# Kernel optimization log

Hardware: AMD Instinct MI355X
Metric: run time of the kernel (lower is better)

Reference implementation:

```python
import jax, jax.numpy as jnp
import numpy as np

G = 8          # deformable groups
K = 9          # 3x3 kernel points
MAXR = 10.0    # max_residue_magnitude


def conv2d(x, w, b):
    # x: [B,Cin,H,W], w: [Cout,Cin,3,3], SAME padding, stride 1
    y = jax.lax.conv_general_dilated(x, w, (1, 1), ((1, 1), (1, 1)),
                                     dimension_numbers=('NCHW', 'OIHW', 'NCHW'))
    return y + b[None, :, None, None]


def lrelu(x):
    return jnp.where(x >= 0, x, 0.1 * x)


def offset_branch(x, ws, bs):
    for w, b in zip(ws[:-1], bs[:-1]):
        x = lrelu(conv2d(x, w, b))
    return conv2d(x, ws[-1], bs[-1])


def mdcn(x, offset, mask, w, b):
    # Modulated deformable conv, 3x3, stride 1, pad 1, dilation 1, groups=1.
    # offset: [B, G*K*2, H, W] ordered (g, k, (y,x)); mask: [B, G*K, H, W]
    B, C, H, W = x.shape
    Cg = C // G
    off = offset.reshape(B, G, K, 2, H, W)
    m = mask.reshape(B, G, K, H, W)
    ky = (jnp.arange(K) // 3 - 1).astype(x.dtype)   # kernel dy, pad=1
    kx = (jnp.arange(K) % 3 - 1).astype(x.dtype)    # kernel dx
    hy = jnp.arange(H, dtype=x.dtype)
    wx = jnp.arange(W, dtype=x.dtype)
    py = hy[None, None, None, :, None] + ky[None, None, :, None, None] + off[:, :, :, 0]  # [B,G,K,H,W]
    px = wx[None, None, None, None, :] + kx[None, None, :, None, None] + off[:, :, :, 1]
    y0f = jnp.floor(py); x0f = jnp.floor(px)
    ly = py - y0f; lx = px - x0f
    y0 = y0f.astype(jnp.int32); x0 = x0f.astype(jnp.int32)
    xf = x.reshape(B, G, Cg, H * W)

    def gather(yi, xi):
        valid = ((yi >= 0) & (yi < H) & (xi >= 0) & (xi < W)).astype(x.dtype)
        yc = jnp.clip(yi, 0, H - 1)
        xc = jnp.clip(xi, 0, W - 1)
        idx = (yc * W + xc).reshape(B, G, 1, K * H * W)
        v = jnp.take_along_axis(xf, idx, axis=3).reshape(B, G, Cg, K, H, W)
        return v * valid.reshape(B, G, 1, K, H, W)

    ly_ = ly[:, :, None]; lx_ = lx[:, :, None]  # [B,G,1,K,H,W]
    samp = (gather(y0, x0) * (1 - ly_) * (1 - lx_)
            + gather(y0, x0 + 1) * (1 - ly_) * lx_
            + gather(y0 + 1, x0) * ly_ * (1 - lx_)
            + gather(y0 + 1, x0 + 1) * ly_ * lx_)
    samp = samp * m[:, :, None]                 # modulation
    wr = w.reshape(w.shape[0], G, Cg, K)        # [Cout,G,Cg,K]
    return jnp.einsum('ogck,bgckhw->bohw', wr, samp) + b[None, :, None, None]


def setup_inputs():
    key = jax.random.key(0)
    ks = jax.random.split(key, 40)
    B, C, H, W = 1, 64, 256, 256
    s = 0.05
    inp = {
        'feat_prev': jax.random.normal(ks[0], (B, C, H, W), jnp.float32),
        'feat_next': jax.random.normal(ks[1], (B, C, H, W), jnp.float32),
        'extra_feat_prev': jax.random.normal(ks[2], (B, 2 * C, H, W), jnp.float32),
        'extra_feat_next': jax.random.normal(ks[3], (B, 2 * C, H, W), jnp.float32),
        'flow_prev': jax.random.normal(ks[4], (B, 2, H, W), jnp.float32),
        'flow_next': jax.random.normal(ks[5], (B, 2, H, W), jnp.float32),
    }
    shapes = [(C, 2 * C, 3, 3), (C, C, 3, 3), (C, C, 3, 3), (27 * G, C, 3, 3)]
    i = 6
    for pre in ('off1', 'off2'):
        for j, sh in enumerate(shapes):
            inp[f'{pre}_w{j}'] = jax.random.normal(ks[i], sh, jnp.float32) * s; i += 1
            inp[f'{pre}_b{j}'] = jax.random.normal(ks[i], (sh[0],), jnp.float32) * s; i += 1
    inp['dcn1_w'] = jax.random.normal(ks[i], (C, C, 3, 3), jnp.float32) * s; i += 1
    inp['dcn1_b'] = jax.random.normal(ks[i], (C,), jnp.float32) * s; i += 1
    inp['dcn2_w'] = jax.random.normal(ks[i], (C, C, 3, 3), jnp.float32) * s; i += 1
    inp['dcn2_b'] = jax.random.normal(ks[i], (C,), jnp.float32) * s; i += 1
    inp['fus_w'] = jax.random.normal(ks[i], (C, 2 * C, 3, 3), jnp.float32) * s; i += 1
    inp['fus_b'] = jax.random.normal(ks[i], (C,), jnp.float32) * s
    return inp


def reference(feat_prev, feat_next, extra_feat_prev, extra_feat_next, flow_prev, flow_next,
              off1_w0, off1_b0, off1_w1, off1_b1, off1_w2, off1_b2, off1_w3, off1_b3,
              off2_w0, off2_b0, off2_w1, off2_b1, off2_w2, off2_b2, off2_w3, off2_b3,
              dcn1_w, dcn1_b, dcn2_w, dcn2_b, fus_w, fus_b):
    def branch(feat, extra, flow, ws, bs, dw, db):
        out = offset_branch(extra, ws, bs)
        o1, o2, msk = jnp.split(out, 3, axis=1)
        off = MAXR * jnp.tanh(jnp.concatenate([o1, o2], axis=1))
        off = off + jnp.tile(flow[:, ::-1], (1, off.shape[1] // 2, 1, 1))  # flip(1).repeat
        msk = jax.nn.sigmoid(msk)
        return mdcn(feat, off, msk, dw, db)

    fp = branch(feat_prev, extra_feat_prev, flow_prev,
                [off1_w0, off1_w1, off1_w2, off1_w3], [off1_b0, off1_b1, off1_b2, off1_b3],
                dcn1_w, dcn1_b)
    fn = branch(feat_next, extra_feat_next, flow_next,
                [off2_w0, off2_w1, off2_w2, off2_w3], [off2_b0, off2_b1, off2_b2, off2_b3],
                dcn2_w, dcn2_b)
    return conv2d(jnp.concatenate([fp, fn], axis=1), fus_w, fus_b)
```

## Files before the change

kernel.cpp:

```cpp
#include <hip/hip_runtime.h>
#include <cstddef>
#include <cstdint>

constexpr int IMG = 256;
constexpr int NPIX = 65536;
constexpr int PW = 258;
constexpr size_t PREC = (size_t)PW * PW;

typedef _Float16 h8 __attribute__((ext_vector_type(8)));
typedef float f32x4 __attribute__((ext_vector_type(4)));

template<int CIN>
__device__ __forceinline__ void zero_pad_rec(int i, _Float16* buf)
{
  constexpr int Q = CIN / 8;
  if (i >= 1028 * Q) return;
  int pr = i / Q, qi = i - pr * Q;
  int rec;
  if (pr < 258) rec = pr;
  else if (pr < 516) rec = 257 * 258 + (pr - 258);
  else { int j = pr - 516; rec = (1 + (j >> 1)) * 258 + ((j & 1) ? 257 : 0); }
  *reinterpret_cast<uint4*>(&buf[(size_t)rec * CIN + qi * 8]) = uint4{0, 0, 0, 0};
}

template<int CIN>
__global__ __launch_bounds__(256) void zeropad_k(_Float16* __restrict__ buf)
{
  zero_pad_rec<CIN>(blockIdx.x * 256 + threadIdx.x, buf);
}

template<int CIN>
__global__ __launch_bounds__(256) void prep_hwc_k(
    const float* __restrict__ in, _Float16* __restrict__ out)
{
  int b = blockIdx.x;
  if (b >= 256) { zero_pad_rec<CIN>((b - 256) * 256 + threadIdx.x, out); return; }
  int pix = b * 256 + threadIdx.x;
  int py = pix >> 8, px = pix & 255;
  size_t rec = ((size_t)(py + 1) * PW + px + 1) * CIN;
#pragma unroll
  for (int c0 = 0; c0 < CIN; c0 += 8) {
    _Float16 t[8];
#pragma unroll
    for (int j = 0; j < 8; ++j)
      t[j] = (_Float16)in[(size_t)(c0 + j) * NPIX + pix];
    *reinterpret_cast<uint4*>(&out[rec + c0]) = *reinterpret_cast<uint4*>(t);
  }
}

__device__ __forceinline__ void wfrag(
    const float* __restrict__ w, int cin_tot, int cin_off, int KC, int NBF,
    int nvalid, int idx, _Float16* __restrict__ oHi, _Float16* __restrict__ oLo)
{
  int l = idx & 63;
  int r = idx >> 6;
  int fg = r % NBF; r /= NBF;
  int c = r % KC;
  int t = r / KC;
  int n = fg * 16 + (l & 15);
  int cinb = c * 32 + (l >> 4) * 8;
  _Float16 vh[8], vl[8];
#pragma unroll
  for (int j = 0; j < 8; ++j) {
    float x = 0.f;
    if (n < nvalid) x = w[((size_t)n * cin_tot + cin_off + cinb + j) * 9 + t];
    vh[j] = (_Float16)x;
    vl[j] = (_Float16)(x - (float)vh[j]);
  }
  *reinterpret_cast<uint4*>(oHi + (size_t)idx * 8) = *reinterpret_cast<uint4*>(vh);
  if (oLo)
    *reinterpret_cast<uint4*>(oLo + (size_t)idx * 8) = *reinterpret_cast<uint4*>(vl);
}

__global__ __launch_bounds__(256) void wprep_all_k(
    const float* __restrict__ w0, const float* __restrict__ w1,
    const float* __restrict__ w2, const float* __restrict__ w3,
    const float* __restrict__ wf, int wf_cin_off, const float* __restrict__ dw,
    _Float16* b0h, _Float16* b0l, _Float16* b1h, _Float16* b1l,
    _Float16* b2h, _Float16* b2l, _Float16* b3h, _Float16* b3l,
    _Float16* bfh, _Float16* __restrict__ wB)
{
  int idx = blockIdx.x * 256 + threadIdx.x;
  if (idx < 9216)       wfrag(w0, 128, 0, 4, 4, 64, idx, b0h, b0l);
  else if (idx < 13824) wfrag(w1, 64, 0, 2, 4, 64, idx - 9216, b1h, b1l);
  else if (idx < 18432) wfrag(w2, 64, 0, 2, 4, 64, idx - 13824, b2h, b2l);
  else if (idx < 36864) wfrag(w3, 64, 0, 2, 16, 216, idx - 18432, b3h, b3l);
  else if (idx < 41472) wfrag(wf, 128, wf_cin_off, 2, 4, 64, idx - 36864, bfh, nullptr);
  else if (idx < 46080) {
    int i = idx - 41472;
    int l = i & 63;
    int r = i >> 6;
    int f = r & 3;
    int p = r >> 2;
    int t = p * 4 + (l >> 4);
    int g = (t * 57) >> 9;
    int k = t - 9 * g;
    int n = f * 16 + (l & 15);
    _Float16 v[8];
#pragma unroll
    for (int j = 0; j < 8; ++j)
      v[j] = (_Float16)dw[(size_t)n * 576 + g * 72 + j * 9 + k];
    *reinterpret_cast<uint4*>(wB + (size_t)i * 8) = *reinterpret_cast<uint4*>(v);
  }
}

template<int CIN, int EPI, bool DBL, typename OT>
__global__ __launch_bounds__(128) void conv_mfma_k(
    const _Float16* __restrict__ act, const _Float16* __restrict__ wHi,
    const _Float16* __restrict__ wLo, const float* __restrict__ bias,
    OT* __restrict__ out, int ncout, int NBF)
{
  constexpr int Q = CIN / 8;
  constexpr int KC = CIN / 32;
  constexpr int NT = DBL ? 2 : 1;
  constexpr int NREC = 198;
  __shared__ __align__(16) _Float16 sA[NREC * CIN];

  const int tid = threadIdx.x;
  const int lane = tid & 63;
  const int wv = tid >> 6;
  const int b = blockIdx.x;
  const int inner = b >> 3;
  const int y = (b & 7) * 32 + (inner & 31);
  const int x0 = (inner >> 5) << 6;
  const int n0 = blockIdx.y << 6;

  for (int i = tid; i < NREC * Q; i += 128) {
    int rec = i / Q, q = i - rec * Q;
    int seg = rec / 66, xr = rec - seg * 66;
    size_t g = ((size_t)(y + seg) * PW + x0 + xr) * CIN + q * 8;
    int slot = (q + rec) & (Q - 1);
    *reinterpret_cast<uint4*>(&sA[rec * CIN + slot * 8]) =
        *reinterpret_cast<const uint4*>(&act[g]);
  }

  const int fgb = (n0 >> 4) + wv * 2;
  auto bload = [&](int t, int c, int nf, const _Float16* src) {
    return *reinterpret_cast<const h8*>(
        &src[((((size_t)t * KC + c) * NBF + fgb + nf) * 64 + lane) * 8]);
  };
  h8 Bn[KC][2][NT];
#pragma unroll
  for (int c = 0; c < KC; ++c)
#pragma unroll
    for (int nf = 0; nf < 2; ++nf) {
      Bn[c][nf][0] = bload(0, c, nf, wHi);
      if (DBL) Bn[c][nf][1] = bload(0, c, nf, wLo);
    }

  f32x4 acc[4][2];
#pragma unroll
  for (int a = 0; a < 4; ++a)
#pragma unroll
    for (int n = 0; n < 2; ++n) acc[a][n] = f32x4{0.f, 0.f, 0.f, 0.f};
  __syncthreads();

  const int m = lane & 15, kq = lane >> 4;
#pragma unroll 1
  for (int t = 0; t < 9; ++t) {
    h8 Bc[KC][2][NT];
#pragma unroll
    for (int c = 0; c < KC; ++c)
#pragma unroll
      for (int nf = 0; nf < 2; ++nf) {
        Bc[c][nf][0] = Bn[c][nf][0];
        if (DBL) Bc[c][nf][1] = Bn[c][nf][1];
      }
    if (t < 8) {
#pragma unroll
      for (int c = 0; c < KC; ++c)
#pragma unroll
        for (int nf = 0; nf < 2; ++nf) {
          Bn[c][nf][0] = bload(t + 1, c, nf, wHi);
          if (DBL) Bn[c][nf][1] = bload(t + 1, c, nf, wLo);
        }
    }
    const int lrb = (t / 3) * 66 + (t % 3) + m;
#pragma unroll
    for (int c = 0; c < KC; ++c) {
      const int q = c * 4 + kq;
#pragma unroll
      for (int mf = 0; mf < 4; ++mf) {
        int lr = lrb + mf * 16;
        int slot = (q + lr) & (Q - 1);
        h8 ah = *reinterpret_cast<const h8*>(&sA[lr * CIN + slot * 8]);
#pragma unroll
        for (int nf = 0; nf < 2; ++nf) {
          acc[mf][nf] = __builtin_amdgcn_mfma_f32_16x16x32_f16(
              ah, Bc[c][nf][0], acc[mf][nf], 0, 0, 0);
          if (DBL)
            acc[mf][nf] = __builtin_amdgcn_mfma_f32_16x16x32_f16(
                ah, Bc[c][nf][1], acc[mf][nf], 0, 0, 0);
        }
      }
    }
  }

  if (EPI == 0) {
#pragma unroll
    for (int nf = 0; nf < 2; ++nf) {
      const int ch = wv * 32 + nf * 16 + m;
      const float bv = bias[ch];
#pragma unroll
      for (int mf = 0; mf < 4; ++mf)
#pragma unroll
        for (int r = 0; r < 4; ++r) {
          int p = mf * 16 + kq * 4 + r;
          float v = acc[mf][nf][r] + bv;
          v = (v >= 0.f) ? v : 0.1f * v;
          reinterpret_cast<_Float16*>(out)[((size_t)(y + 1) * PW + x0 + p + 1) * 64 + ch] =
              (_Float16)v;
        }
    }
  } else {
    __syncthreads();
    float* sF = reinterpret_cast<float*>(sA);
#pragma unroll
    for (int mf = 0; mf < 4; ++mf)
#pragma unroll
      for (int nf = 0; nf < 2; ++nf) {
        int ml = mf * 16 + kq * 4;
        int nl = wv * 32 + nf * 16 + m;
        f32x4 v = acc[mf][nf];
        if (EPI == 1) {
          float bv = (n0 + nl < ncout) ? bias[n0 + nl] : 0.f;
          v[0] += bv; v[1] += bv; v[2] += bv; v[3] += bv;
        }
        *reinterpret_cast<f32x4*>(&sF[nl * 68 + ml]) = v;
      }
    __syncthreads();
    for (int i = tid; i < 1024; i += 128) {
      int row = i >> 4, cx = (i & 15) * 4;
      int gc = n0 + row;
      if (gc < ncout) {
        f32x4 v = *reinterpret_cast<f32x4*>(&sF[row * 68 + cx]);
        size_t ob = (size_t)gc * NPIX + (size_t)y * IMG + x0 + cx;
        if (EPI == 2) {
          float* op = reinterpret_cast<float*>(out) + ob;
          op[0] += v[0]; op[1] += v[1]; op[2] += v[2]; op[3] += v[3];
        } else if (sizeof(OT) == 2) {
          _Float16 t4[4] = {(_Float16)v[0], (_Float16)v[1],
                            (_Float16)v[2], (_Float16)v[3]};
          *reinterpret_cast<uint2*>(reinterpret_cast<_Float16*>(out) + ob) =
              *reinterpret_cast<uint2*>(t4);
        } else {
          *reinterpret_cast<f32x4*>(reinterpret_cast<float*>(out) + ob) = v;
        }
      }
    }
  }
}

__global__ __launch_bounds__(256) void featg_k(
    const float* __restrict__ in, _Float16* __restrict__ out)
{
  int pix = blockIdx.x * 256 + threadIdx.x;
#pragma unroll
  for (int g = 0; g < 8; ++g) {
    _Float16 t[8];
#pragma unroll
    for (int c = 0; c < 8; ++c)
      t[c] = (_Float16)in[(size_t)(g * 8 + c) * NPIX + pix];
    *reinterpret_cast<uint4*>(&out[((size_t)g * NPIX + pix) * 8]) =
        *reinterpret_cast<uint4*>(t);
  }
}

__global__ __launch_bounds__(256, 4) void mdcn_mfma_k(
    const _Float16* __restrict__ featG, const _Float16* __restrict__ o216,
    const float* __restrict__ flow, const _Float16* __restrict__ wB,
    const float* __restrict__ bias, _Float16* __restrict__ actF)
{
  const int tid = threadIdx.x;
  const int lane = tid & 63;
  const int wv = tid >> 6;
  const int b = blockIdx.x;
  const int inner = b >> 3;
  const int row = (b & 7) * 32 + (inner & 31);
  const int xseg = inner >> 5;
  const int m = lane & 15;
  const int tq = lane >> 4;
  const int xw = xseg * 64 + wv * 16;
  const int x = xw + m;
  const int pix = row * 256 + x;

  const float fy = flow[NPIX + pix];
  const float fx = flow[pix];
  const float rowf = (float)row, xf = (float)x;

  f32x4 acc[4];
#pragma unroll
  for (int f = 0; f < 4; ++f) acc[f] = f32x4{0.f, 0.f, 0.f, 0.f};

  auto rawload = [&](int p, float& a0, float& a1, float& a2) {
    int t = p * 4 + tq;
    int g = (t * 57) >> 9;
    int k = t - 9 * g;
    a0 = (float)o216[(size_t)(g * 18 + 2 * k) * NPIX + pix];
    a1 = (float)o216[(size_t)(g * 18 + 2 * k + 1) * NPIX + pix];
    a2 = (float)o216[(size_t)(144 + g * 9 + k) * NPIX + pix];
  };

  auto setup = [&](int p, float s0, float s1, float s2,
                   _Float16& h00, _Float16& h01, _Float16& h10, _Float16& h11,
                   h8& A, h8& B, h8& C, h8& D) {
    const int t = p * 4 + tq;
    const int g = (t * 57) >> 9;
    const int k = t - 9 * g;
    const int kd = (k * 11) >> 5;
    const int km = k - 3 * kd;
    const float mm = __builtin_amdgcn_rcpf(1.f + __expf(-s2));
    const float e0 = __expf(2.f * s0);
    const float e1 = __expf(2.f * s1);
    const float th0 = 1.f - 2.f * __builtin_amdgcn_rcpf(e0 + 1.f);
    const float th1 = 1.f - 2.f * __builtin_amdgcn_rcpf(e1 + 1.f);
    const float pyf = rowf + (float)(kd - 1) + 10.f * th0 + fy;
    const float pxf = xf + (float)(km - 1) + 10.f * th1 + fx;
    const float y0f = floorf(pyf), x0f = floorf(pxf);
    const float ly = pyf - y0f, lx = pxf - x0f;
    const int y0 = (int)y0f, x0i = (int)x0f;
    const int y1 = y0 + 1, x1 = x0i + 1;
    const bool vy0 = (unsigned)y0 < (unsigned)IMG, vy1 = (unsigned)y1 < (unsigned)IMG;
    const bool vx0 = (unsigned)x0i < (unsigned)IMG, vx1 = (unsigned)x1 < (unsigned)IMG;
    const int y0c = min(max(y0, 0), IMG - 1), y1c = min(max(y1, 0), IMG - 1);
    const int x0c = min(max(x0i, 0), IMG - 1), x1c = min(max(x1, 0), IMG - 1);
    const float oy = 1.f - ly, ox = 1.f - lx;
    const float py0 = oy * mm, py1 = ly * mm;
    const float w00 = (vy0 && vx0) ? py0 * ox : 0.f;
    const float w01 = (vy0 && vx1) ? py0 * lx : 0.f;
    const float w10 = (vy1 && vx0) ? py1 * ox : 0.f;
    const float w11 = (vy1 && vx1) ? py1 * lx : 0.f;
    h00 = (_Float16)w00; h01 = (_Float16)w01;
    h10 = (_Float16)w10; h11 = (_Float16)w11;
    const _Float16* fg = featG + ((size_t)g << 19);
    A = *reinterpret_cast<const h8*>(fg + (size_t)(y0c * IMG + x0c) * 8);
    B = *reinterpret_cast<const h8*>(fg + (size_t)(y0c * IMG + x1c) * 8);
    C = *reinterpret_cast<const h8*>(fg + (size_t)(y1c * IMG + x0c) * 8);
    D = *reinterpret_cast<const h8*>(fg + (size_t)(y1c * IMG + x1c) * 8);
  };

  float r0, r1, r2, s0, s1, s2;
  _Float16 h00, h01, h10, h11, v00, v01, v10, v11;
  h8 ga, gb, gc, gd, na, nb, nc, nd;

  rawload(0, s0, s1, s2);
  setup(0, s0, s1, s2, h00, h01, h10, h11, ga, gb, gc, gd);
  rawload(1, r0, r1, r2);

#pragma unroll 1
  for (int p = 0; p < 18; ++p) {
    if (p < 17) setup(p + 1, r0, r1, r2, v00, v01, v10, v11, na, nb, nc, nd);
    if (p < 16) rawload(p + 2, r0, r1, r2);

    const _Float16* wp = wB + ((size_t)p * 256 + lane) * 8;
    h8 bf0 = *reinterpret_cast<const h8*>(wp);
    h8 bf1 = *reinterpret_cast<const h8*>(wp + 512);
    h8 bf2 = *reinterpret_cast<const h8*>(wp + 1024);
    h8 bf3 = *reinterpret_cast<const h8*>(wp + 1536);

    h8 af;
#pragma unroll
    for (int j = 0; j < 8; ++j)
      af[j] = (_Float16)(ga[j] * h00 + gb[j] * h01 + gc[j] * h10 + gd[j] * h11);

    acc[0] = __builtin_amdgcn_mfma_f32_16x16x32_f16(af, bf0, acc[0], 0, 0, 0);
    acc[1] = __builtin_amdgcn_mfma_f32_16x16x32_f16(af, bf1, acc[1], 0, 0, 0);
    acc[2] = __builtin_amdgcn_mfma_f32_16x16x32_f16(af, bf2, acc[2], 0, 0, 0);
    acc[3] = __builtin_amdgcn_mfma_f32_16x16x32_f16(af, bf3, acc[3], 0, 0, 0);

    ga = na; gb = nb; gc = nc; gd = nd;
    h00 = v00; h01 = v01; h10 = v10; h11 = v11;
  }

  const size_t rb = ((size_t)(row + 1) * PW + xw + 1) * 64;
#pragma unroll
  for (int f = 0; f < 4; ++f) {
    const int ch = f * 16 + m;
    const float bv = bias[ch];
#pragma unroll
    for (int r = 0; r < 4; ++r)
      actF[rb + (size_t)(tq * 4 + r) * 64 + ch] = (_Float16)(acc[f][r] + bv);
  }
}

extern "C" void kernel_launch(void* const* d_in, const int* in_sizes, int n_in,
                              void* d_out, int out_size, void* d_ws, size_t ws_size,
                              hipStream_t stream)
{
  const float* feat[2]  = {(const float*)d_in[0], (const float*)d_in[1]};
  const float* extra[2] = {(const float*)d_in[2], (const float*)d_in[3]};
  const float* flow[2]  = {(const float*)d_in[4], (const float*)d_in[5]};
  const float* ow[2][4];
  const float* ob[2][4];
  for (int br = 0; br < 2; ++br)
    for (int j = 0; j < 4; ++j) {
      ow[br][j] = (const float*)d_in[6 + br * 8 + j * 2];
      ob[br][j] = (const float*)d_in[6 + br * 8 + j * 2 + 1];
    }
  const float* dcnw[2] = {(const float*)d_in[22], (const float*)d_in[24]};
  const float* dcnb[2] = {(const float*)d_in[23], (const float*)d_in[25]};
  const float* fusw = (const float*)d_in[26];
  const float* fusb = (const float*)d_in[27];

  char* wsb = (char*)d_ws;
  size_t off = 0;
  auto alloc = [&](size_t bytes) {
    void* p = wsb + off;
    off += (bytes + 255) & ~(size_t)255;
    return p;
  };
  _Float16* actI = (_Float16*)alloc(PREC * 128 * 2);
  _Float16* actA = (_Float16*)alloc(PREC * 64 * 2);
  _Float16* actB = (_Float16*)alloc(PREC * 64 * 2);
  _Float16* actF = (_Float16*)alloc(PREC * 64 * 2);
  _Float16* o216 = (_Float16*)alloc((size_t)216 * NPIX * 2);
  _Float16* featG = (_Float16*)alloc((size_t)8 * NPIX * 8 * 2);
  _Float16* wB = (_Float16*)alloc(36864 * 2);
  _Float16* wb0h = (_Float16*)alloc(147456); _Float16* wb0l = (_Float16*)alloc(147456);
  _Float16* wb1h = (_Float16*)alloc(73728);  _Float16* wb1l = (_Float16*)alloc(73728);
  _Float16* wb2h = (_Float16*)alloc(73728);  _Float16* wb2l = (_Float16*)alloc(73728);
  _Float16* wb3h = (_Float16*)alloc(294912); _Float16* wb3l = (_Float16*)alloc(294912);
  _Float16* wbFh = (_Float16*)alloc(73728);
  float* outp = (float*)d_out;

  dim3 blk256(256), blk128(128);
  zeropad_k<64><<<dim3(33), blk256, 0, stream>>>(actA);
  zeropad_k<64><<<dim3(33), blk256, 0, stream>>>(actB);
  zeropad_k<64><<<dim3(33), blk256, 0, stream>>>(actF);

  for (int br = 0; br < 2; ++br) {
    prep_hwc_k<128><<<dim3(321), blk256, 0, stream>>>(extra[br], actI);
    wprep_all_k<<<dim3(180), blk256, 0, stream>>>(
        ow[br][0], ow[br][1], ow[br][2], ow[br][3], fusw, br * 64, dcnw[br],
        wb0h, wb0l, wb1h, wb1l, wb2h, wb2l, wb3h, wb3l, wbFh, wB);

    conv_mfma_k<128, 0, true, _Float16><<<dim3(1024, 1), blk128, 0, stream>>>(
        actI, wb0h, wb0l, ob[br][0], actA, 64, 4);
    conv_mfma_k<64, 0, true, _Float16><<<dim3(1024, 1), blk128, 0, stream>>>(
        actA, wb1h, wb1l, ob[br][1], actB, 64, 4);
    conv_mfma_k<64, 0, true, _Float16><<<dim3(1024, 1), blk128, 0, stream>>>(
        actB, wb2h, wb2l, ob[br][2], actA, 64, 4);
    conv_mfma_k<64, 1, true, _Float16><<<dim3(1024, 4), blk128, 0, stream>>>(
        actA, wb3h, wb3l, ob[br][3], o216, 216, 16);

    featg_k<<<dim3(256), blk256, 0, stream>>>(feat[br], featG);
    mdcn_mfma_k<<<dim3(1024), blk256, 0, stream>>>(
        featG, o216, flow[br], wB, dcnb[br], actF);

    if (br == 0)
      conv_mfma_k<64, 1, false, float><<<dim3(1024, 1), blk128, 0, stream>>>(
          actF, wbFh, nullptr, fusb, outp, 64, 4);
    else
      conv_mfma_k<64, 2, false, float><<<dim3(1024, 1), blk128, 0, stream>>>(
          actF, wbFh, nullptr, nullptr, outp, 64, 4);
  }
}
```

Measured before the change: 540.8 us.

## Split MDCN reduction over two wave halves with LDS accumulation

Doubles the MDCN block to 512 threads. Each group of four waves handles half of the 18 K-steps (group/kernel-point pairs), and the two partial accumulators are summed through shared memory before the output is written. The goal is more parallelism and latency hiding for the gather-heavy sampling loop, since each wave's serial chain is halved. In exchange it adds an LDS round trip and a block-wide barrier, and the launch bounds of 512 threads with 8 waves per EU may limit register usage.

```diff
diff --git a/kernel.cpp b/kernel.cpp
--- a/kernel.cpp
+++ b/kernel.cpp
@@ -266,23 +266,28 @@
   }
 }
 
-__global__ __launch_bounds__(256, 4) void mdcn_mfma_k(
+__global__ __launch_bounds__(512, 8) void mdcn_mfma_k(
     const _Float16* __restrict__ featG, const _Float16* __restrict__ o216,
     const float* __restrict__ flow, const _Float16* __restrict__ wB,
     const float* __restrict__ bias, _Float16* __restrict__ actF)
 {
+  __shared__ __align__(16) float sRed[4 * 64 * 16];
+
   const int tid = threadIdx.x;
   const int lane = tid & 63;
   const int wv = tid >> 6;
+  const int pg = wv & 3;
+  const int ph = wv >> 2;
   const int b = blockIdx.x;
   const int inner = b >> 3;
   const int row = (b & 7) * 32 + (inner & 31);
   const int xseg = inner >> 5;
   const int m = lane & 15;
   const int tq = lane >> 4;
-  const int xw = xseg * 64 + wv * 16;
+  const int xw = xseg * 64 + pg * 16;
   const int x = xw + m;
   const int pix = row * 256 + x;
+  const int pbase = ph * 9;
 
   const float fy = flow[NPIX + pix];
   const float fx = flow[pix];
@@ -343,14 +348,15 @@
   _Float16 h00, h01, h10, h11, v00, v01, v10, v11;
   h8 ga, gb, gc, gd, na, nb, nc, nd;
 
-  rawload(0, s0, s1, s2);
-  setup(0, s0, s1, s2, h00, h01, h10, h11, ga, gb, gc, gd);
-  rawload(1, r0, r1, r2);
+  rawload(pbase + 0, s0, s1, s2);
+  setup(pbase + 0, s0, s1, s2, h00, h01, h10, h11, ga, gb, gc, gd);
+  rawload(pbase + 1, r0, r1, r2);
 
 #pragma unroll 1
-  for (int p = 0; p < 18; ++p) {
-    if (p < 17) setup(p + 1, r0, r1, r2, v00, v01, v10, v11, na, nb, nc, nd);
-    if (p < 16) rawload(p + 2, r0, r1, r2);
+  for (int i = 0; i < 9; ++i) {
+    const int p = pbase + i;
+    if (i < 8) setup(p + 1, r0, r1, r2, v00, v01, v10, v11, na, nb, nc, nd);
+    if (i < 7) rawload(p + 2, r0, r1, r2);
 
     const _Float16* wp = wB + ((size_t)p * 256 + lane) * 8;
     h8 bf0 = *reinterpret_cast<const h8*>(wp);
@@ -370,6 +376,21 @@
 
     ga = na; gb = nb; gc = nc; gd = nd;
     h00 = v00; h01 = v01; h10 = v10; h11 = v11;
+  }
+
+  if (ph == 1) {
+    float* dst = &sRed[((size_t)(wv - 4) * 64 + lane) * 16];
+#pragma unroll
+    for (int f = 0; f < 4; ++f)
+      *reinterpret_cast<f32x4*>(dst + f * 4) = acc[f];
+  }
+  __syncthreads();
+  if (ph == 1) return;
+  const float* src = &sRed[((size_t)wv * 64 + lane) * 16];
+#pragma unroll
+  for (int f = 0; f < 4; ++f) {
+    f32x4 v = *reinterpret_cast<const f32x4*>(src + f * 4);
+    acc[f][0] += v[0]; acc[f][1] += v[1]; acc[f][2] += v[2]; acc[f][3] += v[3];
   }
 
   const size_t rb = ((size_t)(row + 1) * PW + xw + 1) * 64;
@@ -423,7 +444,7 @@
   _Float16* wbFh = (_Float16*)alloc(73728);
   float* outp = (float*)d_out;
 
-  dim3 blk256(256), blk128(128);
+  dim3 blk256(256), blk128(128), blk512(512);
   zeropad_k<64><<<dim3(33), blk256, 0, stream>>>(actA);
   zeropad_k<64><<<dim3(33), blk256, 0, stream>>>(actB);
   zeropad_k<64><<<dim3(33), blk256, 0, stream>>>(actF);
@@ -444,7 +465,7 @@
         actA, wb3h, wb3l, ob[br][3], o216, 216, 16);
 
     featg_k<<<dim3(256), blk256, 0, stream>>>(feat[br], featG);
-    mdcn_mfma_k<<<dim3(1024), blk256, 0, stream>>>(
+    mdcn_mfma_k<<<dim3(1024), blk512, 0, stream>>>(
         featG, o216, flow[br], wB, dcnb[br], actF);
 
     if (br == 0)
```

Result: slower. 610.2 us (+12.8%).

## Split conv tiles across four waves and double-buffer mdcn loop state

Applied to the files above, without the earlier changes.

The conv kernel now launches 256 threads per block, and each of four waves owns one 16-channel output fragment instead of two. This halves per-wave accumulator and weight registers and gives more waves to hide latency, at the cost of each wave reloading the shared-memory A fragments. The mdcn kernel's software pipeline is rewritten with a ping-pong struct that unrolls by two and prefetches the B weights one iteration ahead, removing the per-iteration register copies. Both changes aim to improve latency hiding and register pressure, with some risk of extra LDS traffic in the conv.

```diff
diff --git a/kernel.cpp b/kernel.cpp
--- a/kernel.cpp
+++ b/kernel.cpp
@@ -105,7 +105,7 @@
 }
 
 template<int CIN, int EPI, bool DBL, typename OT>
-__global__ __launch_bounds__(128) void conv_mfma_k(
+__global__ __launch_bounds__(256) void conv_mfma_k(
     const _Float16* __restrict__ act, const _Float16* __restrict__ wHi,
     const _Float16* __restrict__ wLo, const float* __restrict__ bias,
     OT* __restrict__ out, int ncout, int NBF)
@@ -125,7 +125,7 @@
   const int x0 = (inner >> 5) << 6;
   const int n0 = blockIdx.y << 6;
 
-  for (int i = tid; i < NREC * Q; i += 128) {
+  for (int i = tid; i < NREC * Q; i += 256) {
     int rec = i / Q, q = i - rec * Q;
     int seg = rec / 66, xr = rec - seg * 66;
     size_t g = ((size_t)(y + seg) * PW + x0 + xr) * CIN + q * 8;
@@ -134,46 +134,38 @@
         *reinterpret_cast<const uint4*>(&act[g]);
   }
 
-  const int fgb = (n0 >> 4) + wv * 2;
-  auto bload = [&](int t, int c, int nf, const _Float16* src) {
+  const int fgb = (n0 >> 4) + wv;
+  auto bload = [&](int t, int c, const _Float16* src) {
     return *reinterpret_cast<const h8*>(
-        &src[((((size_t)t * KC + c) * NBF + fgb + nf) * 64 + lane) * 8]);
-  };
-  h8 Bn[KC][2][NT];
-#pragma unroll
-  for (int c = 0; c < KC; ++c)
-#pragma unroll
-    for (int nf = 0; nf < 2; ++nf) {
-      Bn[c][nf][0] = bload(0, c, nf, wHi);
-      if (DBL) Bn[c][nf][1] = bload(0, c, nf, wLo);
-    }
-
-  f32x4 acc[4][2];
-#pragma unroll
-  for (int a = 0; a < 4; ++a)
-#pragma unroll
-    for (int n = 0; n < 2; ++n) acc[a][n] = f32x4{0.f, 0.f, 0.f, 0.f};
+        &src[((((size_t)t * KC + c) * NBF + fgb) * 64 + lane) * 8]);
+  };
+  h8 Bn[KC][NT];
+#pragma unroll
+  for (int c = 0; c < KC; ++c) {
+    Bn[c][0] = bload(0, c, wHi);
+    if (DBL) Bn[c][1] = bload(0, c, wLo);
+  }
+
+  f32x4 acc[4];
+#pragma unroll
+  for (int a = 0; a < 4; ++a) acc[a] = f32x4{0.f, 0.f, 0.f, 0.f};
   __syncthreads();
 
   const int m = lane & 15, kq = lane >> 4;
 #pragma unroll 1
   for (int t = 0; t < 9; ++t) {
-    h8 Bc[KC][2][NT];
-#pragma unroll
-    for (int c = 0; c < KC; ++c)
-#pragma unroll
-      for (int nf = 0; nf < 2; ++nf) {
-        Bc[c][nf][0] = Bn[c][nf][0];
-        if (DBL) Bc[c][nf][1] = Bn[c][nf][1];
+    h8 Bc[KC][NT];
+#pragma unroll
+    for (int c = 0; c < KC; ++c) {
+      Bc[c][0] = Bn[c][0];
+      if (DBL) Bc[c][1] = Bn[c][1];
+    }
+    if (t < 8) {
+#pragma unroll
+      for (int c = 0; c < KC; ++c) {
+        Bn[c][0] = bload(t + 1, c, wHi);
+        if (DBL) Bn[c][1] = bload(t + 1, c, wLo);
       }
-    if (t < 8) {
-#pragma unroll
-      for (int c = 0; c < KC; ++c)
-#pragma unroll
-        for (int nf = 0; nf < 2; ++nf) {
-          Bn[c][nf][0] = bload(t + 1, c, nf, wHi);
-          if (DBL) Bn[c][nf][1] = bload(t + 1, c, nf, wLo);
-        }
     }
     const int lrb = (t / 3) * 66 + (t % 3) + m;
 #pragma unroll
@@ -184,52 +176,44 @@
         int lr = lrb + mf * 16;
         int slot = (q + lr) & (Q - 1);
         h8 ah = *reinterpret_cast<const h8*>(&sA[lr * CIN + slot * 8]);
-#pragma unroll
-        for (int nf = 0; nf < 2; ++nf) {
-          acc[mf][nf] = __builtin_amdgcn_mfma_f32_16x16x32_f16(
-              ah, Bc[c][nf][0], acc[mf][nf], 0, 0, 0);
-          if (DBL)
-            acc[mf][nf] = __builtin_amdgcn_mfma_f32_16x16x32_f16(
-                ah, Bc[c][nf][1], acc[mf][nf], 0, 0, 0);
-        }
+        acc[mf] = __builtin_amdgcn_mfma_f32_16x16x32_f16(
+            ah, Bc[c][0], acc[mf], 0, 0, 0);
+        if (DBL)
+          acc[mf] = __builtin_amdgcn_mfma_f32_16x16x32_f16(
+              ah, Bc[c][1], acc[mf], 0, 0, 0);
       }
     }
   }
 
   if (EPI == 0) {
-#pragma unroll
-    for (int nf = 0; nf < 2; ++nf) {
-      const int ch = wv * 32 + nf * 16 + m;
-      const float bv = bias[ch];
-#pragma unroll
-      for (int mf = 0; mf < 4; ++mf)
-#pragma unroll
-        for (int r = 0; r < 4; ++r) {
-          int p = mf * 16 + kq * 4 + r;
-          float v = acc[mf][nf][r] + bv;
-          v = (v >= 0.f) ? v : 0.1f * v;
-          reinterpret_cast<_Float16*>(out)[((size_t)(y + 1) * PW + x0 + p + 1) * 64 + ch] =
-              (_Float16)v;
-        }
-    }
+    const int ch = wv * 16 + m;
+    const float bv = bias[ch];
+#pragma unroll
+    for (int mf = 0; mf < 4; ++mf)
+#pragma unroll
+      for (int r = 0; r < 4; ++r) {
+        int p = mf * 16 + kq * 4 + r;
+        float v = acc[mf][r] + bv;
+        v = (v >= 0.f) ? v : 0.1f * v;
+        reinterpret_cast<_Float16*>(out)[((size_t)(y + 1) * PW + x0 + p + 1) * 64 + ch] =
+            (_Float16)v;
+      }
   } else {
     __syncthreads();
     float* sF = reinterpret_cast<float*>(sA);
-#pragma unroll
-    for (int mf = 0; mf < 4; ++mf)
-#pragma unroll
-      for (int nf = 0; nf < 2; ++nf) {
-        int ml = mf * 16 + kq * 4;
-        int nl = wv * 32 + nf * 16 + m;
-        f32x4 v = acc[mf][nf];
-        if (EPI == 1) {
-          float bv = (n0 + nl < ncout) ? bias[n0 + nl] : 0.f;
-          v[0] += bv; v[1] += bv; v[2] += bv; v[3] += bv;
-        }
-        *reinterpret_cast<f32x4*>(&sF[nl * 68 + ml]) = v;
+    const int nl = wv * 16 + m;
+#pragma unroll
+    for (int mf = 0; mf < 4; ++mf) {
+      int ml = mf * 16 + kq * 4;
+      f32x4 v = acc[mf];
+      if (EPI == 1) {
+        float bv = (n0 + nl < ncout) ? bias[n0 + nl] : 0.f;
+        v[0] += bv; v[1] += bv; v[2] += bv; v[3] += bv;
       }
+      *reinterpret_cast<f32x4*>(&sF[nl * 68 + ml]) = v;
+    }
     __syncthreads();
-    for (int i = tid; i < 1024; i += 128) {
+    for (int i = tid; i < 1024; i += 256) {
       int row = i >> 4, cx = (i & 15) * 4;
       int gc = n0 + row;
       if (gc < ncout) {
@@ -266,6 +250,13 @@
   }
 }
 
+struct GS {
+  h8 a, b, c, d;
+  _Float16 w00, w01, w10, w11;
+  float r0, r1, r2;
+  h8 bf0, bf1, bf2, bf3;
+};
+
 __global__ __launch_bounds__(256, 4) void mdcn_mfma_k(
     const _Float16* __restrict__ featG, const _Float16* __restrict__ o216,
     const float* __restrict__ flow, const _Float16* __restrict__ wB,
@@ -292,7 +283,7 @@
 #pragma unroll
   for (int f = 0; f < 4; ++f) acc[f] = f32x4{0.f, 0.f, 0.f, 0.f};
 
-  auto rawload = [&](int p, float& a0, float& a1, float& a2) {
+  auto rawloadv = [&](int p, float& a0, float& a1, float& a2) {
     int t = p * 4 + tq;
     int g = (t * 57) >> 9;
     int k = t - 9 * g;
@@ -301,9 +292,7 @@
     a2 = (float)o216[(size_t)(144 + g * 9 + k) * NPIX + pix];
   };
 
-  auto setup = [&](int p, float s0, float s1, float s2,
-                   _Float16& h00, _Float16& h01, _Float16& h10, _Float16& h11,
-                   h8& A, h8& B, h8& C, h8& D) {
+  auto setup = [&](int p, float s0, float s1, float s2, GS& o) {
     const int t = p * 4 + tq;
     const int g = (t * 57) >> 9;
     const int k = t - 9 * g;
@@ -330,47 +319,60 @@
     const float w01 = (vy0 && vx1) ? py0 * lx : 0.f;
     const float w10 = (vy1 && vx0) ? py1 * ox : 0.f;
     const float w11 = (vy1 && vx1) ? py1 * lx : 0.f;
-    h00 = (_Float16)w00; h01 = (_Float16)w01;
-    h10 = (_Float16)w10; h11 = (_Float16)w11;
+    o.w00 = (_Float16)w00; o.w01 = (_Float16)w01;
+    o.w10 = (_Float16)w10; o.w11 = (_Float16)w11;
     const _Float16* fg = featG + ((size_t)g << 19);
-    A = *reinterpret_cast<const h8*>(fg + (size_t)(y0c * IMG + x0c) * 8);
-    B = *reinterpret_cast<const h8*>(fg + (size_t)(y0c * IMG + x1c) * 8);
-    C = *reinterpret_cast<const h8*>(fg + (size_t)(y1c * IMG + x0c) * 8);
-    D = *reinterpret_cast<const h8*>(fg + (size_t)(y1c * IMG + x1c) * 8);
-  };
-
-  float r0, r1, r2, s0, s1, s2;
-  _Float16 h00, h01, h10, h11, v00, v01, v10, v11;
-  h8 ga, gb, gc, gd, na, nb, nc, nd;
-
-  rawload(0, s0, s1, s2);
-  setup(0, s0, s1, s2, h00, h01, h10, h11, ga, gb, gc, gd);
-  rawload(1, r0, r1, r2);
+    o.a = *reinterpret_cast<const h8*>(fg + (size_t)(y0c * IMG + x0c) * 8);
+    o.b = *reinterpret_cast<const h8*>(fg + (size_t)(y0c * IMG + x1c) * 8);
+    o.c = *reinterpret_cast<const h8*>(fg + (size_t)(y1c * IMG + x0c) * 8);
+    o.d = *reinterpret_cast<const h8*>(fg + (size_t)(y1c * IMG + x1c) * 8);
+  };
+
+  auto bfload = [&](int p, GS& o) {
+    const _Float16* wp = wB + ((size_t)p * 256 + lane) * 8;
+    o.bf0 = *reinterpret_cast<const h8*>(wp);
+    o.bf1 = *reinterpret_cast<const h8*>(wp + 512);
+    o.bf2 = *reinterpret_cast<const h8*>(wp + 1024);
+    o.bf3 = *reinterpret_cast<const h8*>(wp + 1536);
+  };
+
+  auto consume = [&](GS& cur) {
+    h8 af;
+#pragma unroll
+    for (int j = 0; j < 8; ++j)
+      af[j] = (_Float16)(cur.a[j] * cur.w00 + cur.b[j] * cur.w01 +
+                         cur.c[j] * cur.w10 + cur.d[j] * cur.w11);
+    acc[0] = __builtin_amdgcn_mfma_f32_16x16x32_f16(af, cur.bf0, acc[0], 0, 0, 0);
+    acc[1] = __builtin_amdgcn_mfma_f32_16x16x32_f16(af, cur.bf1, acc[1], 0, 0, 0);
+    acc[2] = __builtin_amdgcn_mfma_f32_16x16x32_f16(af, cur.bf2, acc[2], 0, 0, 0);
+    acc[3] = __builtin_amdgcn_mfma_f32_16x16x32_f16(af, cur.bf3, acc[3], 0, 0, 0);
+  };
+
+  auto body = [&](int p, GS& cur, GS& nxt) {
+    setup(p + 1, nxt.r0, nxt.r1, nxt.r2, nxt);
+    rawloadv(p + 2, cur.r0, cur.r1, cur.r2);
+    bfload(p + 1, nxt);
+    consume(cur);
+  };
+
+  GS A, B;
+  {
+    float t0, t1, t2;
+    rawloadv(0, t0, t1, t2);
+    rawloadv(1, B.r0, B.r1, B.r2);
+    bfload(0, A);
+    setup(0, t0, t1, t2, A);
+  }
 
 #pragma unroll 1
-  for (int p = 0; p < 18; ++p) {
-    if (p < 17) setup(p + 1, r0, r1, r2, v00, v01, v10, v11, na, nb, nc, nd);
-    if (p < 16) rawload(p + 2, r0, r1, r2);
-
-    const _Float16* wp = wB + ((size_t)p * 256 + lane) * 8;
-    h8 bf0 = *reinterpret_cast<const h8*>(wp);
-    h8 bf1 = *reinterpret_cast<const h8*>(wp + 512);
-    h8 bf2 = *reinterpret_cast<const h8*>(wp + 1024);
-    h8 bf3 = *reinterpret_cast<const h8*>(wp + 1536);
-
-    h8 af;
-#pragma unroll
-    for (int j = 0; j < 8; ++j)
-      af[j] = (_Float16)(ga[j] * h00 + gb[j] * h01 + gc[j] * h10 + gd[j] * h11);
-
-    acc[0] = __builtin_amdgcn_mfma_f32_16x16x32_f16(af, bf0, acc[0], 0, 0, 0);
-    acc[1] = __builtin_amdgcn_mfma_f32_16x16x32_f16(af, bf1, acc[1], 0, 0, 0);
-    acc[2] = __builtin_amdgcn_mfma_f32_16x16x32_f16(af, bf2, acc[2], 0, 0, 0);
-    acc[3] = __builtin_amdgcn_mfma_f32_16x16x32_f16(af, bf3, acc[3], 0, 0, 0);
-
-    ga = na; gb = nb; gc = nc; gd = nd;
-    h00 = v00; h01 = v01; h10 = v10; h11 = v11;
-  }
+  for (int it = 0; it < 8; ++it) {
+    body(2 * it, A, B);
+    body(2 * it + 1, B, A);
+  }
+  setup(17, B.r0, B.r1, B.r2, B);
+  bfload(17, B);
+  consume(A);
+  consume(B);
 
   const size_t rb = ((size_t)(row + 1) * PW + xw + 1) * 64;
 #pragma unroll
@@ -423,7 +425,7 @@
   _Float16* wbFh = (_Float16*)alloc(73728);
   float* outp = (float*)d_out;
 
-  dim3 blk256(256), blk128(128);
+  dim3 blk256(256);
   zeropad_k<64><<<dim3(33), blk256, 0, stream>>>(actA);
   zeropad_k<64><<<dim3(33), blk256, 0, stream>>>(actB);
   zeropad_k<64><<<dim3(33), blk256, 0, stream>>>(actF);
@@ -434,13 +436,13 @@
         ow[br][0], ow[br][1], ow[br][2], ow[br][3], fusw, br * 64, dcnw[br],
         wb0h, wb0l, wb1h, wb1l, wb2h, wb2l, wb3h, wb3l, wbFh, wB);
 
-    conv_mfma_k<128, 0, true, _Float16><<<dim3(1024, 1), blk128, 0, stream>>>(
+    conv_mfma_k<128, 0, true, _Float16><<<dim3(1024, 1), blk256, 0, stream>>>(
         actI, wb0h, wb0l, ob[br][0], actA, 64, 4);
-    conv_mfma_k<64, 0, true, _Float16><<<dim3(1024, 1), blk128, 0, stream>>>(
+    conv_mfma_k<64, 0, true, _Float16><<<dim3(1024, 1), blk256, 0, stream>>>(
         actA, wb1h, wb1l, ob[br][1], actB, 64, 4);
-    conv_mfma_k<64, 0, true, _Float16><<<dim3(1024, 1), blk128, 0, stream>>>(
+    conv_mfma_k<64, 0, true, _Float16><<<dim3(1024, 1), blk256, 0, stream>>>(
         actB, wb2h, wb2l, ob[br][2], actA, 64, 4);
-    conv_mfma_k<64, 1, true, _Float16><<<dim3(1024, 4), blk128, 0, stream>>>(
+    conv_mfma_k<64, 1, true, _Float16><<<dim3(1024, 4), blk256, 0, stream>>>(
         actA, wb3h, wb3l, ob[br][3], o216, 216, 16);
 
     featg_k<<<dim3(256), blk256, 0, stream>>>(feat[br], featG);
@@ -448,10 +450,10 @@
         featG, o216, flow[br], wB, dcnb[br], actF);
 
     if (br == 0)
-      conv_mfma_k<64, 1, false, float><<<dim3(1024, 1), blk128, 0, stream>>>(
+      conv_mfma_k<64, 1, false, float><<<dim3(1024, 1), blk256, 0, stream>>>(
           actF, wbFh, nullptr, fusb, outp, 64, 4);
     else
-      conv_mfma_k<64, 2, false, float><<<dim3(1024, 1), blk128, 0, stream>>>(
+      conv_mfma_k<64, 2, false, float><<<dim3(1024, 1), blk256, 0, stream>>>(
           actF, wbFh, nullptr, nullptr, outp, 64, 4);
   }
 }
```

Measured after the change: 515.8 us. -4.6%, faster.
